# Optimization experiments

Hardware: AMD Instinct MI355X
Metric: run time of the kernel (lower is better)

The kernel has to match this reference:

```python
import jax, jax.numpy as jnp
import numpy as np

TOP_K = 2

def setup_inputs() -> dict:
    key = jax.random.key(0)
    k1, k2, k3, k4 = jax.random.split(key, 4)
    N, H, F, E = 2048, 1024, 2048, 8
    x = jax.random.normal(k1, (N, H), dtype=jnp.float32)
    router_weight = jax.random.normal(k2, (H, E), dtype=jnp.float32) * 0.02
    w1 = jax.random.normal(k3, (E, H, F), dtype=jnp.float32) * 0.02
    w2 = jax.random.normal(k4, (E, F, H), dtype=jnp.float32) * 0.02
    return {"x": x, "router_weight": router_weight, "w1": w1, "w2": w2}

def reference(x, router_weight, w1, w2):
    # Router: softmax over experts, top-k, renormalize (matches torch forward).
    N = x.shape[0]
    E = router_weight.shape[1]
    logits = x.astype(jnp.float32) @ router_weight            # [N, E]
    rprobs = jax.nn.softmax(logits, axis=-1)
    topk_p, topk_i = jax.lax.top_k(rprobs, TOP_K)             # [N, K]
    topk_p = topk_p / jnp.sum(topk_p, axis=-1, keepdims=True)
    # Scatter normalized top-k probs into dense [N, E] gate matrix; zeros
    # everywhere else, so gating subsumes the boolean routing_map.
    probs = jnp.zeros((N, E), dtype=jnp.float32).at[
        jnp.arange(N)[:, None], topk_i].set(topk_p)
    # Expert FFN (same math as permute -> grouped GEMM -> weighted scatter-add:
    # out[t] = sum_e probs[t,e] * gelu(x[t] @ w1[e]) @ w2[e]).
    h = jnp.einsum('nh,ehf->enf', x, w1)                      # [E, N, F]
    h = jax.nn.gelu(h, approximate=False)                     # torch F.gelu is erf-based
    y = jnp.einsum('enf,efh->enh', h, w2)                     # [E, N, H]
    out = jnp.einsum('enh,ne->nh', y, probs.astype(x.dtype))  # weighted combine
    return out
```

## Files before the change

### kernel.cpp

```cpp
#include <hip/hip_runtime.h>
#include <hip/hip_fp16.h>
#include <math.h>

#define NTOK 2048
#define HID  1024
#define FFN  2048
#define NEXP 8

#define BM 128
#define BN 128
#define BK 32
#define MAX_TILES 40
#define TLDA 66

#define WS_COUNTS 0
#define WS_SEG    32
#define WS_PROBS  128
#define WS_LISTS  (128 + NTOK*NEXP*4)
#define WS_XH     262144
#define WS_W1T    (WS_XH + NTOK*HID*2)
#define WS_W2T    (WS_W1T + NEXP*HID*FFN*2)
#define WS_HBUF   (WS_W2T + NEXP*HID*FFN*2)

typedef _Float16 half8 __attribute__((ext_vector_type(8)));
typedef float    f32x4 __attribute__((ext_vector_type(4)));

static __device__ __forceinline__ unsigned short f2h_bits(float f) {
  union { _Float16 h; unsigned short u; } v;
  v.h = (_Float16)f;
  return v.u;
}
static __device__ __forceinline__ unsigned pack2(float a, float b) {
  return (unsigned)f2h_bits(a) | ((unsigned)f2h_bits(b) << 16);
}

#define GLOAD16(gsrc, ldst) \
  __builtin_amdgcn_global_load_lds( \
      (const __attribute__((address_space(1))) unsigned int*)(gsrc), \
      (__attribute__((address_space(3))) unsigned int*)(ldst), 16, 0, 0)

#define VMCNT0 asm volatile("s_waitcnt vmcnt(0)" ::: "memory")

__global__ __launch_bounds__(256) void moe_prep(
    const float* __restrict__ x, const float* __restrict__ rw,
    const float* __restrict__ w1, const float* __restrict__ w2,
    unsigned short* __restrict__ xh, unsigned short* __restrict__ w1t,
    unsigned short* __restrict__ w2t,
    int* __restrict__ counts, int* __restrict__ lists, float* __restrict__ probs)
{
  __shared__ unsigned short Ls[64 * TLDA];
  const int bid = blockIdx.x;
  const int tid = threadIdx.x;

  if (bid < 8192) {
    const float* src; unsigned short* dst; int C, R, r0, c0;
    if (bid < 4096) {
      const int e = bid >> 9, rem = bid & 511;
      R = HID; C = FFN;
      r0 = (rem >> 5) * 64; c0 = (rem & 31) * 64;
      src = w1 + (size_t)e * HID * FFN;
      dst = w1t + (size_t)e * HID * FFN;
    } else {
      const int u = bid - 4096;
      const int e = u >> 9, rem = u & 511;
      R = FFN; C = HID;
      r0 = (rem >> 4) * 64; c0 = (rem & 15) * 64;
      src = w2 + (size_t)e * HID * FFN;
      dst = w2t + (size_t)e * HID * FFN;
    }
    {
      const int row = tid >> 2, cq = tid & 3;
      const float4* sp = reinterpret_cast<const float4*>(
          src + (size_t)(r0 + row) * C + c0 + cq * 16);
      float4 a = sp[0], b = sp[1], c = sp[2], d = sp[3];
      unsigned pk[8] = {pack2(a.x,a.y), pack2(a.z,a.w), pack2(b.x,b.y), pack2(b.z,b.w),
                        pack2(c.x,c.y), pack2(c.z,c.w), pack2(d.x,d.y), pack2(d.z,d.w)};
      unsigned* Ld = reinterpret_cast<unsigned*>(Ls);
      const int dbase = row * (TLDA/2) + cq * 8;
#pragma unroll
      for (int j = 0; j < 8; ++j) Ld[dbase + j] = pk[j];
    }
    __syncthreads();
    {
      const int c = tid >> 2, rs = tid & 3;
      unsigned v[8];
#pragma unroll
      for (int j = 0; j < 8; ++j) {
        unsigned lo = Ls[(rs*16 + 2*j    ) * TLDA + c];
        unsigned hi = Ls[(rs*16 + 2*j + 1) * TLDA + c];
        v[j] = lo | (hi << 16);
      }
      unsigned short* dp = dst + (size_t)(c0 + c) * R + r0 + rs * 16;
      *reinterpret_cast<uint4*>(dp)     = (uint4){v[0], v[1], v[2], v[3]};
      *reinterpret_cast<uint4*>(dp + 8) = (uint4){v[4], v[5], v[6], v[7]};
    }
  } else {
    const int wid = tid >> 6, lane = tid & 63;
    const int t = (bid - 8192) * 4 + wid;
    const float* xr = x + (size_t)t * HID + lane * 16;
    const float4* xp = reinterpret_cast<const float4*>(xr);
    float4 v0 = xp[0], v1 = xp[1], v2 = xp[2], v3 = xp[3];
    float xv[16] = {v0.x,v0.y,v0.z,v0.w, v1.x,v1.y,v1.z,v1.w,
                    v2.x,v2.y,v2.z,v2.w, v3.x,v3.y,v3.z,v3.w};
    float acc[NEXP];
#pragma unroll
    for (int e = 0; e < NEXP; ++e) acc[e] = 0.f;
#pragma unroll
    for (int j = 0; j < 16; ++j) {
      const float4* rp = reinterpret_cast<const float4*>(rw + (size_t)(lane*16 + j) * NEXP);
      float4 a = rp[0], b = rp[1];
      acc[0] += xv[j]*a.x; acc[1] += xv[j]*a.y; acc[2] += xv[j]*a.z; acc[3] += xv[j]*a.w;
      acc[4] += xv[j]*b.x; acc[5] += xv[j]*b.y; acc[6] += xv[j]*b.z; acc[7] += xv[j]*b.w;
    }
#pragma unroll
    for (int off = 32; off > 0; off >>= 1) {
#pragma unroll
      for (int e = 0; e < NEXP; ++e) acc[e] += __shfl_down(acc[e], off);
    }
    unsigned short* xd = xh + (size_t)t * HID + lane * 16;
    *reinterpret_cast<uint4*>(xd) =
        (uint4){pack2(v0.x,v0.y), pack2(v0.z,v0.w), pack2(v1.x,v1.y), pack2(v1.z,v1.w)};
    *reinterpret_cast<uint4*>(xd + 8) =
        (uint4){pack2(v2.x,v2.y), pack2(v2.z,v2.w), pack2(v3.x,v3.y), pack2(v3.z,v3.w)};
    if (lane == 0) {
      float m = acc[0];
#pragma unroll
      for (int e = 1; e < NEXP; ++e) m = fmaxf(m, acc[e]);
      float p[NEXP];
#pragma unroll
      for (int e = 0; e < NEXP; ++e) p[e] = expf(acc[e] - m);
      int i0 = 0;
#pragma unroll
      for (int e = 1; e < NEXP; ++e) if (p[e] > p[i0]) i0 = e;
      int i1 = -1;
#pragma unroll
      for (int e = 0; e < NEXP; ++e) {
        if (e == i0) continue;
        if (i1 < 0 || p[e] > p[i1]) i1 = e;
      }
      const float inv = 1.f / (p[i0] + p[i1]);
      probs[t * NEXP + i0] = p[i0] * inv;
      probs[t * NEXP + i1] = p[i1] * inv;
      int pos0 = atomicAdd(&counts[i0], 1); lists[i0 * NTOK + pos0] = t;
      int pos1 = atomicAdd(&counts[i1], 1); lists[i1 * NTOK + pos1] = t;
    }
  }
}

__global__ void moe_segoff(const int* __restrict__ counts, int* __restrict__ seg) {
  if (threadIdx.x == 0 && blockIdx.x == 0) {
    int run = 0;
    for (int e = 0; e < NEXP; ++e) {
      seg[e] = run;
      run += ((counts[e] + BM - 1) / BM) * BM;
    }
    seg[NEXP] = run;
  }
}

__global__ __launch_bounds__(256) void moe_gemm1(
    const unsigned short* __restrict__ xh, const unsigned short* __restrict__ w1t,
    const int* __restrict__ counts, const int* __restrict__ seg,
    const int* __restrict__ lists, unsigned short* __restrict__ hbuf)
{
  const int tile = blockIdx.x >> 4;
  const int jcol = blockIdx.x & 15;
  const int rb = tile * BM;
  if (rb >= seg[NEXP]) return;
  int e = 0;
#pragma unroll
  for (int q = 1; q < NEXP; ++q) if (seg[q] <= rb) e = q;
  const int cnt = counts[e];
  const int rloc0 = rb - seg[e];

  __shared__ int tokL[BM];
  __shared__ __align__(16) unsigned short Asm[2][BM*BK];
  __shared__ __align__(16) unsigned short Bsm[2][BM*BK];

  const int tid = threadIdx.x;
  if (tid < BM) {
    int rl = rloc0 + tid;
    tokL[tid] = (rl < cnt) ? lists[e * NTOK + rl] : 0;
  }
  __syncthreads();

  const int lane = tid & 63;
  const int wid = tid >> 6;
  const int wr = (wid >> 1) * 64;
  const int wc = (wid & 1) * 64;
  const int lr = (lane >> 4) * 4;
  const int lc = lane & 15;
  const int khi = (lane >> 4) * 8;

  const int cw8 = (lane & 3) * 8;
  const int r0 = wid*16 + (lane >> 2);
  const unsigned short* abase[2];
  const unsigned short* bbase[2];
  abase[0] = xh + (size_t)tokL[r0]      * HID + cw8;
  abase[1] = xh + (size_t)tokL[64 + r0] * HID + cw8;
  bbase[0] = w1t + ((size_t)e * FFN + jcol*BN + r0)      * HID + cw8;
  bbase[1] = w1t + ((size_t)e * FFN + jcol*BN + 64 + r0) * HID + cw8;

  f32x4 acc[4][4];
#pragma unroll
  for (int m = 0; m < 4; ++m)
#pragma unroll
    for (int n = 0; n < 4; ++n)
      acc[m][n] = (f32x4){0.f, 0.f, 0.f, 0.f};

#define STAGE1(buf, kk) do { \
    _Pragma("unroll") \
    for (int i = 0; i < 2; ++i) { \
      GLOAD16(abase[i] + (kk), &Asm[buf][(i*256 + wid*64)*8]); \
      GLOAD16(bbase[i] + (kk), &Bsm[buf][(i*256 + wid*64)*8]); \
    } } while (0)

  STAGE1(0, 0);
  VMCNT0;
  __syncthreads();
  int cur = 0;
  for (int kk = 0; kk < HID; kk += BK) {
    if (kk + BK < HID) STAGE1(cur ^ 1, kk + BK);
    half8 af[4], bf[4];
#pragma unroll
    for (int m = 0; m < 4; ++m)
      af[m] = *reinterpret_cast<const half8*>(&Asm[cur][(wr + m*16 + lc)*BK + khi]);
#pragma unroll
    for (int n = 0; n < 4; ++n)
      bf[n] = *reinterpret_cast<const half8*>(&Bsm[cur][(wc + n*16 + lc)*BK + khi]);
#pragma unroll
    for (int m = 0; m < 4; ++m)
#pragma unroll
      for (int n = 0; n < 4; ++n)
        acc[m][n] = __builtin_amdgcn_mfma_f32_16x16x32_f16(af[m], bf[n], acc[m][n], 0, 0, 0);
    VMCNT0;
    __syncthreads();
    cur ^= 1;
  }
#undef STAGE1

#pragma unroll
  for (int m = 0; m < 4; ++m) {
#pragma unroll
    for (int r = 0; r < 4; ++r) {
      unsigned short* hp = hbuf + (size_t)(rb + wr + m*16 + lr + r) * FFN + jcol*BN + wc + lc;
#pragma unroll
      for (int n = 0; n < 4; ++n) {
        float v = acc[m][n][r];
        float g = 0.5f * v * (1.f + erff(v * 0.70710678118f));
        hp[n*16] = f2h_bits(g);
      }
    }
  }
}

__global__ __launch_bounds__(256) void moe_gemm2(
    const unsigned short* __restrict__ hbuf, const unsigned short* __restrict__ w2t,
    const int* __restrict__ counts, const int* __restrict__ seg,
    const int* __restrict__ lists, const float* __restrict__ probs,
    float* __restrict__ out)
{
  const int tile = blockIdx.x >> 4;
  const int jcol = (blockIdx.x >> 1) & 7;
  const int ks   = blockIdx.x & 1;
  const int rb = tile * BM;
  if (rb >= seg[NEXP]) return;
  int e = 0;
#pragma unroll
  for (int q = 1; q < NEXP; ++q) if (seg[q] <= rb) e = q;
  const int cnt = counts[e];
  const int rloc0 = rb - seg[e];
  const int k0 = ks * (FFN / 2);
  const int k1 = k0 + (FFN / 2);

  __shared__ int tokL[BM];
  __shared__ float pL[BM];
  __shared__ __align__(16) unsigned short Asm[2][BM*BK];
  __shared__ __align__(16) unsigned short Bsm[2][BM*BK];

  const int tid = threadIdx.x;
  if (tid < BM) {
    int rl = rloc0 + tid;
    if (rl < cnt) {
      int tk = lists[e * NTOK + rl];
      tokL[tid] = tk;
      pL[tid] = probs[tk * NEXP + e];
    } else { tokL[tid] = 0; pL[tid] = 0.f; }
  }
  __syncthreads();

  const int lane = tid & 63;
  const int wid = tid >> 6;
  const int wr = (wid >> 1) * 64;
  const int wc = (wid & 1) * 64;
  const int lr = (lane >> 4) * 4;
  const int lc = lane & 15;
  const int khi = (lane >> 4) * 8;

  const int cw8 = (lane & 3) * 8;
  const int r0 = wid*16 + (lane >> 2);
  const unsigned short* abase[2];
  const unsigned short* bbase[2];
  abase[0] = hbuf + (size_t)(rb + r0)      * FFN + cw8;
  abase[1] = hbuf + (size_t)(rb + 64 + r0) * FFN + cw8;
  bbase[0] = w2t + ((size_t)e * HID + jcol*BN + r0)      * FFN + cw8;
  bbase[1] = w2t + ((size_t)e * HID + jcol*BN + 64 + r0) * FFN + cw8;

  f32x4 acc[4][4];
#pragma unroll
  for (int m = 0; m < 4; ++m)
#pragma unroll
    for (int n = 0; n < 4; ++n)
      acc[m][n] = (f32x4){0.f, 0.f, 0.f, 0.f};

#define STAGE2(buf, kk) do { \
    _Pragma("unroll") \
    for (int i = 0; i < 2; ++i) { \
      GLOAD16(abase[i] + (kk), &Asm[buf][(i*256 + wid*64)*8]); \
      GLOAD16(bbase[i] + (kk), &Bsm[buf][(i*256 + wid*64)*8]); \
    } } while (0)

  STAGE2(0, k0);
  VMCNT0;
  __syncthreads();
  int cur = 0;
  for (int kk = k0; kk < k1; kk += BK) {
    if (kk + BK < k1) STAGE2(cur ^ 1, kk + BK);
    half8 af[4], bf[4];
#pragma unroll
    for (int m = 0; m < 4; ++m)
      af[m] = *reinterpret_cast<const half8*>(&Asm[cur][(wr + m*16 + lc)*BK + khi]);
#pragma unroll
    for (int n = 0; n < 4; ++n)
      bf[n] = *reinterpret_cast<const half8*>(&Bsm[cur][(wc + n*16 + lc)*BK + khi]);
#pragma unroll
    for (int m = 0; m < 4; ++m)
#pragma unroll
      for (int n = 0; n < 4; ++n)
        acc[m][n] = __builtin_amdgcn_mfma_f32_16x16x32_f16(af[m], bf[n], acc[m][n], 0, 0, 0);
    VMCNT0;
    __syncthreads();
    cur ^= 1;
  }
#undef STAGE2

#pragma unroll
  for (int m = 0; m < 4; ++m) {
#pragma unroll
    for (int r = 0; r < 4; ++r) {
      const int lrow = wr + m*16 + lr + r;
      const int rl = rloc0 + lrow;
      if (rl >= cnt) continue;
      const int tok = tokL[lrow];
      const float p = pL[lrow];
      float* op = out + (size_t)tok * HID + jcol*BN + wc + lc;
#pragma unroll
      for (int n = 0; n < 4; ++n)
        atomicAdd(&op[n*16], p * acc[m][n][r]);
    }
  }
}

extern "C" void kernel_launch(void* const* d_in, const int* in_sizes, int n_in,
                              void* d_out, int out_size, void* d_ws, size_t ws_size,
                              hipStream_t stream) {
  const float* x  = (const float*)d_in[0];
  const float* rw = (const float*)d_in[1];
  const float* w1 = (const float*)d_in[2];
  const float* w2 = (const float*)d_in[3];
  float* out = (float*)d_out;

  char* ws = (char*)d_ws;
  int*   counts = (int*)(ws + WS_COUNTS);
  int*   seg    = (int*)(ws + WS_SEG);
  float* probs  = (float*)(ws + WS_PROBS);
  int*   lists  = (int*)(ws + WS_LISTS);
  unsigned short* xh   = (unsigned short*)(ws + WS_XH);
  unsigned short* w1t  = (unsigned short*)(ws + WS_W1T);
  unsigned short* w2t  = (unsigned short*)(ws + WS_W2T);
  unsigned short* hbuf = (unsigned short*)(ws + WS_HBUF);

  hipMemsetAsync(ws, 0, 128, stream);
  hipMemsetAsync(d_out, 0, (size_t)NTOK * HID * sizeof(float), stream);

  moe_prep<<<8192 + NTOK/4, 256, 0, stream>>>(x, rw, w1, w2, xh, w1t, w2t,
                                              counts, lists, probs);
  moe_segoff<<<1, 64, 0, stream>>>(counts, seg);
  moe_gemm1<<<MAX_TILES * (FFN / BN), 256, 0, stream>>>(xh, w1t, counts, seg, lists, hbuf);
  moe_gemm2<<<MAX_TILES * (HID / BN) * 2, 256, 0, stream>>>(hbuf, w2t, counts, seg, lists, probs, out);
}
```

Baseline: 191.6 us.

## Overlap w2 transpose with first GEMM and batch four tiles per transpose block

The w2 fp32-to-fp16 transpose is moved out of the prep kernel and appended as extra blocks of the first grouped GEMM kernel, so its memory traffic runs alongside GEMM1's compute. Each transpose block now handles four 64x64 tiles with double-buffered LDS and register prefetch of the next tile, which cuts the block count and hides load latency. The cost is a larger GEMM1 grid whose transpose blocks compete with GEMM tiles for CUs, and a shared LDS buffer that is reinterpreted between the two roles.

```diff
diff --git a/kernel.cpp b/kernel.cpp
--- a/kernel.cpp
+++ b/kernel.cpp
@@ -41,109 +41,131 @@
 
 #define VMCNT0 asm volatile("s_waitcnt vmcnt(0)" ::: "memory")
 
-__global__ __launch_bounds__(256) void moe_prep(
+template<int IS_W1>
+static __device__ __forceinline__ void transpose4(
+    int t0, const float* __restrict__ wsrc, unsigned short* __restrict__ wdst,
+    unsigned short (*Ls)[64*TLDA], int tid)
+{
+  const int row = tid >> 2, cq = tid & 3;
+  const int oc  = tid >> 2, rs = tid & 3;
+  const int e = t0 >> 9;
+  const int R = IS_W1 ? HID : FFN;
+  const int C = IS_W1 ? FFN : HID;
+  const float* src = wsrc + (size_t)e * HID * FFN;
+  unsigned short* dst = wdst + (size_t)e * HID * FFN;
+  float4 ld[2][4];
+
+#define TGEOM(tt, r0v, c0v) \
+    { const int rem_ = (t0 + (tt)) & 511; \
+      r0v = IS_W1 ? ((rem_ >> 5) * 64) : ((rem_ >> 4) * 64); \
+      c0v = IS_W1 ? ((rem_ & 31) * 64) : ((rem_ & 15) * 64); }
+
+  {
+    int r0, c0; TGEOM(0, r0, c0);
+    const float4* sp = reinterpret_cast<const float4*>(
+        src + (size_t)(r0 + row) * C + c0 + cq * 16);
+#pragma unroll
+    for (int j = 0; j < 4; ++j) ld[0][j] = sp[j];
+  }
+#pragma unroll
+  for (int t = 0; t < 4; ++t) {
+    if (t < 3) {
+      int r0, c0; TGEOM(t + 1, r0, c0);
+      const float4* sp = reinterpret_cast<const float4*>(
+          src + (size_t)(r0 + row) * C + c0 + cq * 16);
+#pragma unroll
+      for (int j = 0; j < 4; ++j) ld[(t + 1) & 1][j] = sp[j];
+    }
+    {
+      unsigned* Ld = reinterpret_cast<unsigned*>(Ls[t & 1]);
+      const int dbase = row * (TLDA / 2) + cq * 8;
+      const float4 a = ld[t & 1][0], b = ld[t & 1][1];
+      const float4 c2 = ld[t & 1][2], d = ld[t & 1][3];
+      Ld[dbase + 0] = pack2(a.x, a.y);  Ld[dbase + 1] = pack2(a.z, a.w);
+      Ld[dbase + 2] = pack2(b.x, b.y);  Ld[dbase + 3] = pack2(b.z, b.w);
+      Ld[dbase + 4] = pack2(c2.x, c2.y); Ld[dbase + 5] = pack2(c2.z, c2.w);
+      Ld[dbase + 6] = pack2(d.x, d.y);  Ld[dbase + 7] = pack2(d.z, d.w);
+    }
+    __syncthreads();
+    {
+      int r0, c0; TGEOM(t, r0, c0);
+      unsigned v[8];
+#pragma unroll
+      for (int j = 0; j < 8; ++j) {
+        unsigned lo = Ls[t & 1][(rs * 16 + 2 * j    ) * TLDA + oc];
+        unsigned hi = Ls[t & 1][(rs * 16 + 2 * j + 1) * TLDA + oc];
+        v[j] = lo | (hi << 16);
+      }
+      unsigned short* dp = dst + (size_t)(c0 + oc) * R + r0 + rs * 16;
+      *reinterpret_cast<uint4*>(dp)     = (uint4){v[0], v[1], v[2], v[3]};
+      *reinterpret_cast<uint4*>(dp + 8) = (uint4){v[4], v[5], v[6], v[7]};
+    }
+  }
+#undef TGEOM
+}
+
+__global__ __launch_bounds__(256) void moe_prep1(
     const float* __restrict__ x, const float* __restrict__ rw,
-    const float* __restrict__ w1, const float* __restrict__ w2,
+    const float* __restrict__ w1,
     unsigned short* __restrict__ xh, unsigned short* __restrict__ w1t,
-    unsigned short* __restrict__ w2t,
     int* __restrict__ counts, int* __restrict__ lists, float* __restrict__ probs)
 {
-  __shared__ unsigned short Ls[64 * TLDA];
+  __shared__ unsigned short Ls[2][64 * TLDA];
   const int bid = blockIdx.x;
   const int tid = threadIdx.x;
 
-  if (bid < 8192) {
-    const float* src; unsigned short* dst; int C, R, r0, c0;
-    if (bid < 4096) {
-      const int e = bid >> 9, rem = bid & 511;
-      R = HID; C = FFN;
-      r0 = (rem >> 5) * 64; c0 = (rem & 31) * 64;
-      src = w1 + (size_t)e * HID * FFN;
-      dst = w1t + (size_t)e * HID * FFN;
-    } else {
-      const int u = bid - 4096;
-      const int e = u >> 9, rem = u & 511;
-      R = FFN; C = HID;
-      r0 = (rem >> 4) * 64; c0 = (rem & 15) * 64;
-      src = w2 + (size_t)e * HID * FFN;
-      dst = w2t + (size_t)e * HID * FFN;
-    }
-    {
-      const int row = tid >> 2, cq = tid & 3;
-      const float4* sp = reinterpret_cast<const float4*>(
-          src + (size_t)(r0 + row) * C + c0 + cq * 16);
-      float4 a = sp[0], b = sp[1], c = sp[2], d = sp[3];
-      unsigned pk[8] = {pack2(a.x,a.y), pack2(a.z,a.w), pack2(b.x,b.y), pack2(b.z,b.w),
-                        pack2(c.x,c.y), pack2(c.z,c.w), pack2(d.x,d.y), pack2(d.z,d.w)};
-      unsigned* Ld = reinterpret_cast<unsigned*>(Ls);
-      const int dbase = row * (TLDA/2) + cq * 8;
-#pragma unroll
-      for (int j = 0; j < 8; ++j) Ld[dbase + j] = pk[j];
-    }
-    __syncthreads();
-    {
-      const int c = tid >> 2, rs = tid & 3;
-      unsigned v[8];
-#pragma unroll
-      for (int j = 0; j < 8; ++j) {
-        unsigned lo = Ls[(rs*16 + 2*j    ) * TLDA + c];
-        unsigned hi = Ls[(rs*16 + 2*j + 1) * TLDA + c];
-        v[j] = lo | (hi << 16);
-      }
-      unsigned short* dp = dst + (size_t)(c0 + c) * R + r0 + rs * 16;
-      *reinterpret_cast<uint4*>(dp)     = (uint4){v[0], v[1], v[2], v[3]};
-      *reinterpret_cast<uint4*>(dp + 8) = (uint4){v[4], v[5], v[6], v[7]};
-    }
-  } else {
-    const int wid = tid >> 6, lane = tid & 63;
-    const int t = (bid - 8192) * 4 + wid;
-    const float* xr = x + (size_t)t * HID + lane * 16;
-    const float4* xp = reinterpret_cast<const float4*>(xr);
-    float4 v0 = xp[0], v1 = xp[1], v2 = xp[2], v3 = xp[3];
-    float xv[16] = {v0.x,v0.y,v0.z,v0.w, v1.x,v1.y,v1.z,v1.w,
-                    v2.x,v2.y,v2.z,v2.w, v3.x,v3.y,v3.z,v3.w};
-    float acc[NEXP];
-#pragma unroll
-    for (int e = 0; e < NEXP; ++e) acc[e] = 0.f;
-#pragma unroll
-    for (int j = 0; j < 16; ++j) {
-      const float4* rp = reinterpret_cast<const float4*>(rw + (size_t)(lane*16 + j) * NEXP);
-      float4 a = rp[0], b = rp[1];
-      acc[0] += xv[j]*a.x; acc[1] += xv[j]*a.y; acc[2] += xv[j]*a.z; acc[3] += xv[j]*a.w;
-      acc[4] += xv[j]*b.x; acc[5] += xv[j]*b.y; acc[6] += xv[j]*b.z; acc[7] += xv[j]*b.w;
-    }
-#pragma unroll
-    for (int off = 32; off > 0; off >>= 1) {
-#pragma unroll
-      for (int e = 0; e < NEXP; ++e) acc[e] += __shfl_down(acc[e], off);
-    }
-    unsigned short* xd = xh + (size_t)t * HID + lane * 16;
-    *reinterpret_cast<uint4*>(xd) =
-        (uint4){pack2(v0.x,v0.y), pack2(v0.z,v0.w), pack2(v1.x,v1.y), pack2(v1.z,v1.w)};
-    *reinterpret_cast<uint4*>(xd + 8) =
-        (uint4){pack2(v2.x,v2.y), pack2(v2.z,v2.w), pack2(v3.x,v3.y), pack2(v3.z,v3.w)};
-    if (lane == 0) {
-      float m = acc[0];
-#pragma unroll
-      for (int e = 1; e < NEXP; ++e) m = fmaxf(m, acc[e]);
-      float p[NEXP];
-#pragma unroll
-      for (int e = 0; e < NEXP; ++e) p[e] = expf(acc[e] - m);
-      int i0 = 0;
-#pragma unroll
-      for (int e = 1; e < NEXP; ++e) if (p[e] > p[i0]) i0 = e;
-      int i1 = -1;
-#pragma unroll
-      for (int e = 0; e < NEXP; ++e) {
-        if (e == i0) continue;
-        if (i1 < 0 || p[e] > p[i1]) i1 = e;
-      }
-      const float inv = 1.f / (p[i0] + p[i1]);
-      probs[t * NEXP + i0] = p[i0] * inv;
-      probs[t * NEXP + i1] = p[i1] * inv;
-      int pos0 = atomicAdd(&counts[i0], 1); lists[i0 * NTOK + pos0] = t;
-      int pos1 = atomicAdd(&counts[i1], 1); lists[i1 * NTOK + pos1] = t;
-    }
+  if (bid < 1024) {
+    transpose4<1>(bid * 4, w1, w1t, Ls, tid);
+    return;
+  }
+  const int wid = tid >> 6, lane = tid & 63;
+  const int t = (bid - 1024) * 4 + wid;
+  const float* xr = x + (size_t)t * HID + lane * 16;
+  const float4* xp = reinterpret_cast<const float4*>(xr);
+  float4 v0 = xp[0], v1 = xp[1], v2 = xp[2], v3 = xp[3];
+  float xv[16] = {v0.x,v0.y,v0.z,v0.w, v1.x,v1.y,v1.z,v1.w,
+                  v2.x,v2.y,v2.z,v2.w, v3.x,v3.y,v3.z,v3.w};
+  float acc[NEXP];
+#pragma unroll
+  for (int e = 0; e < NEXP; ++e) acc[e] = 0.f;
+#pragma unroll
+  for (int j = 0; j < 16; ++j) {
+    const float4* rp = reinterpret_cast<const float4*>(rw + (size_t)(lane*16 + j) * NEXP);
+    float4 a = rp[0], b = rp[1];
+    acc[0] += xv[j]*a.x; acc[1] += xv[j]*a.y; acc[2] += xv[j]*a.z; acc[3] += xv[j]*a.w;
+    acc[4] += xv[j]*b.x; acc[5] += xv[j]*b.y; acc[6] += xv[j]*b.z; acc[7] += xv[j]*b.w;
+  }
+#pragma unroll
+  for (int off = 32; off > 0; off >>= 1) {
+#pragma unroll
+    for (int e = 0; e < NEXP; ++e) acc[e] += __shfl_down(acc[e], off);
+  }
+  unsigned short* xd = xh + (size_t)t * HID + lane * 16;
+  *reinterpret_cast<uint4*>(xd) =
+      (uint4){pack2(v0.x,v0.y), pack2(v0.z,v0.w), pack2(v1.x,v1.y), pack2(v1.z,v1.w)};
+  *reinterpret_cast<uint4*>(xd + 8) =
+      (uint4){pack2(v2.x,v2.y), pack2(v2.z,v2.w), pack2(v3.x,v3.y), pack2(v3.z,v3.w)};
+  if (lane == 0) {
+    float m = acc[0];
+#pragma unroll
+    for (int e = 1; e < NEXP; ++e) m = fmaxf(m, acc[e]);
+    float p[NEXP];
+#pragma unroll
+    for (int e = 0; e < NEXP; ++e) p[e] = expf(acc[e] - m);
+    int i0 = 0;
+#pragma unroll
+    for (int e = 1; e < NEXP; ++e) if (p[e] > p[i0]) i0 = e;
+    int i1 = -1;
+#pragma unroll
+    for (int e = 0; e < NEXP; ++e) {
+      if (e == i0) continue;
+      if (i1 < 0 || p[e] > p[i1]) i1 = e;
+    }
+    const float inv = 1.f / (p[i0] + p[i1]);
+    probs[t * NEXP + i0] = p[i0] * inv;
+    probs[t * NEXP + i1] = p[i1] * inv;
+    int pos0 = atomicAdd(&counts[i0], 1); lists[i0 * NTOK + pos0] = t;
+    int pos1 = atomicAdd(&counts[i1], 1); lists[i1 * NTOK + pos1] = t;
   }
 }
 
@@ -158,13 +180,25 @@
   }
 }
 
-__global__ __launch_bounds__(256) void moe_gemm1(
+__global__ __launch_bounds__(256) void moe_k2(
     const unsigned short* __restrict__ xh, const unsigned short* __restrict__ w1t,
+    const float* __restrict__ w2, unsigned short* __restrict__ w2t,
     const int* __restrict__ counts, const int* __restrict__ seg,
     const int* __restrict__ lists, unsigned short* __restrict__ hbuf)
 {
-  const int tile = blockIdx.x >> 4;
-  const int jcol = blockIdx.x & 15;
+  __shared__ __align__(16) unsigned short SMEM[4 * BM * BK];
+  __shared__ int tokL[BM];
+  const int bid = blockIdx.x;
+  const int tid = threadIdx.x;
+
+  if (bid >= MAX_TILES * 16) {
+    transpose4<0>((bid - MAX_TILES * 16) * 4, w2, w2t,
+                  reinterpret_cast<unsigned short(*)[64 * TLDA]>(SMEM), tid);
+    return;
+  }
+
+  const int tile = bid >> 4;
+  const int jcol = bid & 15;
   const int rb = tile * BM;
   if (rb >= seg[NEXP]) return;
   int e = 0;
@@ -173,11 +207,9 @@
   const int cnt = counts[e];
   const int rloc0 = rb - seg[e];
 
-  __shared__ int tokL[BM];
-  __shared__ __align__(16) unsigned short Asm[2][BM*BK];
-  __shared__ __align__(16) unsigned short Bsm[2][BM*BK];
-
-  const int tid = threadIdx.x;
+  unsigned short (*Asm)[BM*BK] = reinterpret_cast<unsigned short(*)[BM*BK]>(SMEM);
+  unsigned short (*Bsm)[BM*BK] = reinterpret_cast<unsigned short(*)[BM*BK]>(SMEM + 2*BM*BK);
+
   if (tid < BM) {
     int rl = rloc0 + tid;
     tokL[tid] = (rl < cnt) ? lists[e * NTOK + rl] : 0;
@@ -383,9 +415,10 @@
   hipMemsetAsync(ws, 0, 128, stream);
   hipMemsetAsync(d_out, 0, (size_t)NTOK * HID * sizeof(float), stream);
 
-  moe_prep<<<8192 + NTOK/4, 256, 0, stream>>>(x, rw, w1, w2, xh, w1t, w2t,
-                                              counts, lists, probs);
+  moe_prep1<<<1024 + NTOK/4, 256, 0, stream>>>(x, rw, w1, xh, w1t,
+                                               counts, lists, probs);
   moe_segoff<<<1, 64, 0, stream>>>(counts, seg);
-  moe_gemm1<<<MAX_TILES * (FFN / BN), 256, 0, stream>>>(xh, w1t, counts, seg, lists, hbuf);
+  moe_k2<<<MAX_TILES * 16 + 1024, 256, 0, stream>>>(xh, w1t, w2, w2t,
+                                                    counts, seg, lists, hbuf);
   moe_gemm2<<<MAX_TILES * (HID / BN) * 2, 256, 0, stream>>>(hbuf, w2t, counts, seg, lists, probs, out);
 }
```

After: 184.6 us. 1.04x faster.
